# Optimization experiments

Hardware: AMD Instinct MI355X
Metric: run time of the kernel (lower is better)

Reference implementation:

```python
import jax, jax.numpy as jnp
import numpy as np

N1, N2, D = 8192, 8192, 128

def setup_inputs() -> dict:
    key = jax.random.key(0)
    k1, k2, k3, k4 = jax.random.split(key, 4)
    X1 = jax.random.normal(k1, (N1, D), dtype=jnp.float32)
    X2 = jax.random.normal(k2, (N2, D), dtype=jnp.float32)
    task1 = jax.random.randint(k3, (N1,), 0, 2, dtype=jnp.int32)
    task2 = jax.random.randint(k4, (N2,), 0, 2, dtype=jnp.int32)
    # learned parameters (init values match module defaults: lengthscale=1, output_variance=1, b=0)
    log_l = jnp.zeros((D,), dtype=jnp.float32)          # log(1)
    log_theta_l = jnp.zeros((1,), dtype=jnp.float32)    # log(1)
    b = jnp.zeros((1,), dtype=jnp.float32)
    return {"X1": X1, "X2": X2, "log_l": log_l, "log_theta_l": log_theta_l,
            "b": b, "task1": task1, "task2": task2}

def reference(X1, X2, log_l, log_theta_l, b, task1, task2):
    l = jnp.exp(log_l)                      # (D,) ARD lengthscales
    A = X1 / l                              # (N1, D)
    B = X2 / l                              # (N2, D)
    # sum((a-b)^2) = |a|^2 + |b|^2 - 2 a.b  -> GEMM form, no (N1,N2,D) intermediate
    sq_dist = (jnp.sum(A * A, axis=1)[:, None]
               + jnp.sum(B * B, axis=1)[None, :]
               - 2.0 * (A @ B.T))
    sq_dist = jnp.maximum(sq_dist, 0.0)
    K_base = jnp.exp(log_theta_l[0]) * jnp.exp(-0.5 * sq_dist)   # (N1, N2)
    # lambda = clip(2/(1+exp(b)) - 1, 0, 1)
    lam = jnp.clip(2.0 / (1.0 + jnp.exp(b[0])) - 1.0, 0.0, 1.0)
    diff_task = task1[:, None] != task2[None, :]                 # (N1, N2) bool
    K = K_base * jnp.where(diff_task, lam, 1.0)
    return K
```

## Files before the change

kernel.cpp:

```cpp
#include <hip/hip_runtime.h>
#include <stdint.h>

typedef float f32x4 __attribute__((ext_vector_type(4)));
typedef __bf16 bf16x8 __attribute__((ext_vector_type(8)));

#define N1 8192
#define N2 8192
#define DD 128
#define BK 32

__device__ __forceinline__ void gload_lds16(const void* g, void* l) {
    __builtin_amdgcn_global_load_lds(
        (const __attribute__((address_space(1))) uint32_t*)g,
        (__attribute__((address_space(3))) uint32_t*)l,
        16, 0, 0);
}

__global__ __launch_bounds__(256) void tgp_kernel(
    const float* __restrict__ X1, const float* __restrict__ X2,
    const float* __restrict__ log_l,
    const float* __restrict__ log_theta_l, const float* __restrict__ bparam,
    const int* __restrict__ t1, const int* __restrict__ t2,
    float* __restrict__ C)
{
    __shared__ __align__(128) char smem[65536 + 1536];
    float* const bounce = (float*)smem;
    float* const ils = (float*)(smem + 65536);
    float* const n1s = ils + 128;
    float* const n2s = ils + 256;

    const int t = threadIdx.x;
    const int lane = t & 63;
    const int wave = t >> 6;
    const int wr = wave >> 1, wc = wave & 1;
    const int lr = lane & 15, lg = lane >> 4;

    int wg = blockIdx.x;
    int swz = (wg & 7) * 512 + (wg >> 3);
    int tm = swz >> 6, tn = swz & 63;

    const float* Ag = X1 + (size_t)(tm * 128) * DD;
    const float* Bg = X2 + (size_t)(tn * 128) * DD;

    f32x4 acc[4][4];
    #pragma unroll
    for (int i = 0; i < 4; ++i)
        #pragma unroll
        for (int j = 0; j < 4; ++j) acc[i][j] = (f32x4){0.f, 0.f, 0.f, 0.f};

    #define STAGE(buf, kt)                                                          \
    {                                                                               \
        char* lb = smem + (buf) * 32768;                                            \
        int slot, row, ul;                                                          \
        slot = t;       row = slot >> 3; ul = (slot & 7) ^ (row & 7);               \
        gload_lds16(Ag + (size_t)row * DD + (kt) * BK + ul * 4, lb + slot * 16);    \
        gload_lds16(Bg + (size_t)row * DD + (kt) * BK + ul * 4, lb + 16384 + slot * 16); \
        slot = t + 256; row = slot >> 3; ul = (slot & 7) ^ (row & 7);               \
        gload_lds16(Ag + (size_t)row * DD + (kt) * BK + ul * 4, lb + slot * 16);    \
        gload_lds16(Bg + (size_t)row * DD + (kt) * BK + ul * 4, lb + 16384 + slot * 16); \
        slot = t + 512; row = slot >> 3; ul = (slot & 7) ^ (row & 7);               \
        gload_lds16(Ag + (size_t)row * DD + (kt) * BK + ul * 4, lb + slot * 16);    \
        gload_lds16(Bg + (size_t)row * DD + (kt) * BK + ul * 4, lb + 16384 + slot * 16); \
        slot = t + 768; row = slot >> 3; ul = (slot & 7) ^ (row & 7);               \
        gload_lds16(Ag + (size_t)row * DD + (kt) * BK + ul * 4, lb + slot * 16);    \
        gload_lds16(Bg + (size_t)row * DD + (kt) * BK + ul * 4, lb + 16384 + slot * 16); \
    }

    STAGE(0, 0);
    if (t < 128) ils[t] = __expf(-log_l[t]);
    __syncthreads();

    float nrm_acc = 0.f;
    const int nrow = t & 127;
    const int nroff = (t < 128) ? 0 : 16384;
    int cur = 0;

    for (int kt = 0; kt < 4; ++kt) {
        if (kt < 3) STAGE(cur ^ 1, kt + 1);

        const float* tA = (const float*)(smem + cur * 32768);
        const float* tB = tA + 4096;

        {
            const float* tp = (const float*)(smem + cur * 32768 + nroff);
            #pragma unroll
            for (int u = 0; u < 8; ++u) {
                int up = u ^ (nrow & 7);
                f32x4 x = *(const f32x4*)(tp + nrow * 32 + up * 4);
                f32x4 il = *(const f32x4*)(ils + kt * 32 + u * 4);
                f32x4 sx = x * il;
                nrm_acc += sx[0]*sx[0] + sx[1]*sx[1] + sx[2]*sx[2] + sx[3]*sx[3];
            }
        }

        float il8[8];
        {
            f32x4 i0 = *(const f32x4*)(ils + kt * 32 + lg * 8);
            f32x4 i1 = *(const f32x4*)(ils + kt * 32 + lg * 8 + 4);
            il8[0]=i0[0]; il8[1]=i0[1]; il8[2]=i0[2]; il8[3]=i0[3];
            il8[4]=i1[0]; il8[5]=i1[1]; il8[6]=i1[2]; il8[7]=i1[3];
        }
        bf16x8 ah[4], al[4], bh[4], bl[4];
        #pragma unroll
        for (int mi = 0; mi < 4; ++mi) {
            int row = wr * 64 + mi * 16 + lr;
            int p0 = (2 * lg) ^ (row & 7), p1 = (2 * lg + 1) ^ (row & 7);
            f32x4 x0 = *(const f32x4*)(tA + row * 32 + p0 * 4);
            f32x4 x1 = *(const f32x4*)(tA + row * 32 + p1 * 4);
            float sv[8] = {x0[0]*il8[0], x0[1]*il8[1], x0[2]*il8[2], x0[3]*il8[3],
                           x1[0]*il8[4], x1[1]*il8[5], x1[2]*il8[6], x1[3]*il8[7]};
            #pragma unroll
            for (int e = 0; e < 8; ++e) {
                __bf16 h = (__bf16)sv[e];
                ah[mi][e] = h;
                al[mi][e] = (__bf16)(sv[e] - (float)h);
            }
        }
        #pragma unroll
        for (int ni = 0; ni < 4; ++ni) {
            int row = wc * 64 + ni * 16 + lr;
            int p0 = (2 * lg) ^ (row & 7), p1 = (2 * lg + 1) ^ (row & 7);
            f32x4 x0 = *(const f32x4*)(tB + row * 32 + p0 * 4);
            f32x4 x1 = *(const f32x4*)(tB + row * 32 + p1 * 4);
            float sv[8] = {x0[0]*il8[0], x0[1]*il8[1], x0[2]*il8[2], x0[3]*il8[3],
                           x1[0]*il8[4], x1[1]*il8[5], x1[2]*il8[6], x1[3]*il8[7]};
            #pragma unroll
            for (int e = 0; e < 8; ++e) {
                __bf16 h = (__bf16)sv[e];
                bh[ni][e] = h;
                bl[ni][e] = (__bf16)(sv[e] - (float)h);
            }
        }

        #pragma unroll
        for (int mi = 0; mi < 4; ++mi)
            #pragma unroll
            for (int ni = 0; ni < 4; ++ni) {
                acc[mi][ni] = __builtin_amdgcn_mfma_f32_16x16x32_bf16(bh[ni], ah[mi], acc[mi][ni], 0, 0, 0);
                acc[mi][ni] = __builtin_amdgcn_mfma_f32_16x16x32_bf16(bh[ni], al[mi], acc[mi][ni], 0, 0, 0);
                acc[mi][ni] = __builtin_amdgcn_mfma_f32_16x16x32_bf16(bl[ni], ah[mi], acc[mi][ni], 0, 0, 0);
            }
        __syncthreads();
        cur ^= 1;
    }
    #undef STAGE

    if (t < 128) n1s[t] = nrm_acc; else n2s[t - 128] = nrm_acc;
    __syncthreads();

    float logt = log_theta_l[0];
    float bb = bparam[0];
    float lam = fminf(fmaxf(2.f / (1.f + __expf(bb)) - 1.f, 0.f), 1.f);
    int rbase = tm * 128, cbase = tn * 128;

    #pragma unroll
    for (int mi = 0; mi < 4; ++mi) {
        int rowl = wr * 64 + mi * 16 + lr;
        float n1v = n1s[rowl];
        int t1v = t1[rbase + rowl];
        #pragma unroll
        for (int ni = 0; ni < 4; ++ni) {
            int coll = wc * 64 + ni * 16 + lg * 4;
            f32x4 kv;
            #pragma unroll
            for (int r = 0; r < 4; ++r) {
                float dot = acc[mi][ni][r];
                float n2v = n2s[coll + r];
                int t2v = t2[cbase + coll + r];
                float s = fmaxf(n1v + n2v - 2.f * dot, 0.f);
                float k = __expf(fmaf(-0.5f, s, logt));
                if (t1v != t2v) k *= lam;
                kv[r] = k;
            }
            int phys = rowl * 128 + (coll ^ ((rowl & 7) << 2));
            *(f32x4*)(bounce + phys) = kv;
        }
    }
    __syncthreads();

    #pragma unroll
    for (int s2 = 0; s2 < 16; ++s2) {
        int lrow = s2 * 8 + (t >> 5);
        int lcol = (t & 31) * 4;
        int phys = lrow * 128 + (lcol ^ ((lrow & 7) << 2));
        f32x4 v = *(const f32x4*)(bounce + phys);
        *(f32x4*)(C + (size_t)(rbase + lrow) * N2 + (cbase + lcol)) = v;
    }
}

extern "C" void kernel_launch(void* const* d_in, const int* in_sizes, int n_in,
                              void* d_out, int out_size, void* d_ws, size_t ws_size,
                              hipStream_t stream)
{
    const float* X1 = (const float*)d_in[0];
    const float* X2 = (const float*)d_in[1];
    const float* log_l = (const float*)d_in[2];
    const float* log_theta = (const float*)d_in[3];
    const float* bp = (const float*)d_in[4];
    const int* t1 = (const int*)d_in[5];
    const int* t2 = (const int*)d_in[6];
    float* C = (float*)d_out;
    (void)d_ws; (void)ws_size; (void)in_sizes; (void)n_in; (void)out_size;

    tgp_kernel<<<4096, 256, 0, stream>>>(X1, X2, log_l, log_theta, bp, t1, t2, C);
}
```

Measured before the change: 117.5 us.

## Drop LDS staging; load operands directly from global and store output directly

Removes the double-buffered global-to-LDS async staging and the LDS bounce buffer used for coalesced output writes. Operands are now read straight from global into registers, row norms are computed per lane and reduced with wave shuffles, and results are written directly to global in MFMA layout. LDS use drops to a few hundred bytes and launch bounds request 3 blocks per SM, trading coalesced 512-byte row stores for 16-byte scattered stores and losing load/compute overlap.

```diff
diff --git a/kernel.cpp b/kernel.cpp
--- a/kernel.cpp
+++ b/kernel.cpp
@@ -4,43 +4,35 @@
 typedef float f32x4 __attribute__((ext_vector_type(4)));
 typedef __bf16 bf16x8 __attribute__((ext_vector_type(8)));
 
-#define N1 8192
-#define N2 8192
-#define DD 128
-#define BK 32
+#define NN 8192
+#define DDIM 128
 
-__device__ __forceinline__ void gload_lds16(const void* g, void* l) {
-    __builtin_amdgcn_global_load_lds(
-        (const __attribute__((address_space(1))) uint32_t*)g,
-        (__attribute__((address_space(3))) uint32_t*)l,
-        16, 0, 0);
-}
-
-__global__ __launch_bounds__(256) void tgp_kernel(
+__global__ __launch_bounds__(256, 3) void tgp_kernel(
     const float* __restrict__ X1, const float* __restrict__ X2,
     const float* __restrict__ log_l,
     const float* __restrict__ log_theta_l, const float* __restrict__ bparam,
-    const int* __restrict__ t1, const int* __restrict__ t2,
+    const int* __restrict__ task1, const int* __restrict__ task2,
     float* __restrict__ C)
 {
-    __shared__ __align__(128) char smem[65536 + 1536];
-    float* const bounce = (float*)smem;
-    float* const ils = (float*)(smem + 65536);
-    float* const n1s = ils + 128;
-    float* const n2s = ils + 256;
+    __shared__ float ils[128];
+    __shared__ float n1s[128];
+    __shared__ float n2s[128];
 
     const int t = threadIdx.x;
     const int lane = t & 63;
-    const int wave = t >> 6;
-    const int wr = wave >> 1, wc = wave & 1;
+    const int wv = t >> 6;
+    const int wr = wv >> 1, wc = wv & 1;
     const int lr = lane & 15, lg = lane >> 4;
 
     int wg = blockIdx.x;
     int swz = (wg & 7) * 512 + (wg >> 3);
     int tm = swz >> 6, tn = swz & 63;
 
-    const float* Ag = X1 + (size_t)(tm * 128) * DD;
-    const float* Bg = X2 + (size_t)(tn * 128) * DD;
+    const float* Ag = X1 + (size_t)tm * 128 * DDIM;
+    const float* Bg = X2 + (size_t)tn * 128 * DDIM;
+
+    if (t < 128) ils[t] = __expf(-log_l[t]);
+    __syncthreads();
 
     f32x4 acc[4][4];
     #pragma unroll
@@ -48,87 +40,50 @@
         #pragma unroll
         for (int j = 0; j < 4; ++j) acc[i][j] = (f32x4){0.f, 0.f, 0.f, 0.f};
 
-    #define STAGE(buf, kt)                                                          \
-    {                                                                               \
-        char* lb = smem + (buf) * 32768;                                            \
-        int slot, row, ul;                                                          \
-        slot = t;       row = slot >> 3; ul = (slot & 7) ^ (row & 7);               \
-        gload_lds16(Ag + (size_t)row * DD + (kt) * BK + ul * 4, lb + slot * 16);    \
-        gload_lds16(Bg + (size_t)row * DD + (kt) * BK + ul * 4, lb + 16384 + slot * 16); \
-        slot = t + 256; row = slot >> 3; ul = (slot & 7) ^ (row & 7);               \
-        gload_lds16(Ag + (size_t)row * DD + (kt) * BK + ul * 4, lb + slot * 16);    \
-        gload_lds16(Bg + (size_t)row * DD + (kt) * BK + ul * 4, lb + 16384 + slot * 16); \
-        slot = t + 512; row = slot >> 3; ul = (slot & 7) ^ (row & 7);               \
-        gload_lds16(Ag + (size_t)row * DD + (kt) * BK + ul * 4, lb + slot * 16);    \
-        gload_lds16(Bg + (size_t)row * DD + (kt) * BK + ul * 4, lb + 16384 + slot * 16); \
-        slot = t + 768; row = slot >> 3; ul = (slot & 7) ^ (row & 7);               \
-        gload_lds16(Ag + (size_t)row * DD + (kt) * BK + ul * 4, lb + slot * 16);    \
-        gload_lds16(Bg + (size_t)row * DD + (kt) * BK + ul * 4, lb + 16384 + slot * 16); \
-    }
+    float nA[4] = {0.f, 0.f, 0.f, 0.f};
+    float nB[4] = {0.f, 0.f, 0.f, 0.f};
 
-    STAGE(0, 0);
-    if (t < 128) ils[t] = __expf(-log_l[t]);
-    __syncthreads();
+    #pragma unroll
+    for (int c = 0; c < 4; ++c) {
+        f32x4 il0 = *(const f32x4*)(ils + c * 32 + lg * 8);
+        f32x4 il1 = *(const f32x4*)(ils + c * 32 + lg * 8 + 4);
 
-    float nrm_acc = 0.f;
-    const int nrow = t & 127;
-    const int nroff = (t < 128) ? 0 : 16384;
-    int cur = 0;
+        bf16x8 ah[4], al[4], bh[4], bl[4];
 
-    for (int kt = 0; kt < 4; ++kt) {
-        if (kt < 3) STAGE(cur ^ 1, kt + 1);
-
-        const float* tA = (const float*)(smem + cur * 32768);
-        const float* tB = tA + 4096;
-
-        {
-            const float* tp = (const float*)(smem + cur * 32768 + nroff);
-            #pragma unroll
-            for (int u = 0; u < 8; ++u) {
-                int up = u ^ (nrow & 7);
-                f32x4 x = *(const f32x4*)(tp + nrow * 32 + up * 4);
-                f32x4 il = *(const f32x4*)(ils + kt * 32 + u * 4);
-                f32x4 sx = x * il;
-                nrm_acc += sx[0]*sx[0] + sx[1]*sx[1] + sx[2]*sx[2] + sx[3]*sx[3];
-            }
-        }
-
-        float il8[8];
-        {
-            f32x4 i0 = *(const f32x4*)(ils + kt * 32 + lg * 8);
-            f32x4 i1 = *(const f32x4*)(ils + kt * 32 + lg * 8 + 4);
-            il8[0]=i0[0]; il8[1]=i0[1]; il8[2]=i0[2]; il8[3]=i0[3];
-            il8[4]=i1[0]; il8[5]=i1[1]; il8[6]=i1[2]; il8[7]=i1[3];
-        }
-        bf16x8 ah[4], al[4], bh[4], bl[4];
         #pragma unroll
         for (int mi = 0; mi < 4; ++mi) {
-            int row = wr * 64 + mi * 16 + lr;
-            int p0 = (2 * lg) ^ (row & 7), p1 = (2 * lg + 1) ^ (row & 7);
-            f32x4 x0 = *(const f32x4*)(tA + row * 32 + p0 * 4);
-            f32x4 x1 = *(const f32x4*)(tA + row * 32 + p1 * 4);
-            float sv[8] = {x0[0]*il8[0], x0[1]*il8[1], x0[2]*il8[2], x0[3]*il8[3],
-                           x1[0]*il8[4], x1[1]*il8[5], x1[2]*il8[6], x1[3]*il8[7]};
+            const float* p = Ag + (size_t)(wr * 64 + mi * 16 + lr) * DDIM + c * 32 + lg * 8;
+            f32x4 x0 = *(const f32x4*)p;
+            f32x4 x1 = *(const f32x4*)(p + 4);
+            x0 *= il0; x1 *= il1;
+            nA[mi] += x0[0]*x0[0] + x0[1]*x0[1] + x0[2]*x0[2] + x0[3]*x0[3]
+                    + x1[0]*x1[0] + x1[1]*x1[1] + x1[2]*x1[2] + x1[3]*x1[3];
             #pragma unroll
-            for (int e = 0; e < 8; ++e) {
-                __bf16 h = (__bf16)sv[e];
-                ah[mi][e] = h;
-                al[mi][e] = (__bf16)(sv[e] - (float)h);
+            for (int e = 0; e < 4; ++e) {
+                __bf16 h0 = (__bf16)x0[e];
+                ah[mi][e] = h0;
+                al[mi][e] = (__bf16)(x0[e] - (float)h0);
+                __bf16 h1 = (__bf16)x1[e];
+                ah[mi][e + 4] = h1;
+                al[mi][e + 4] = (__bf16)(x1[e] - (float)h1);
             }
         }
         #pragma unroll
         for (int ni = 0; ni < 4; ++ni) {
-            int row = wc * 64 + ni * 16 + lr;
-            int p0 = (2 * lg) ^ (row & 7), p1 = (2 * lg + 1) ^ (row & 7);
-            f32x4 x0 = *(const f32x4*)(tB + row * 32 + p0 * 4);
-            f32x4 x1 = *(const f32x4*)(tB + row * 32 + p1 * 4);
-            float sv[8] = {x0[0]*il8[0], x0[1]*il8[1], x0[2]*il8[2], x0[3]*il8[3],
-                           x1[0]*il8[4], x1[1]*il8[5], x1[2]*il8[6], x1[3]*il8[7]};
+            const float* p = Bg + (size_t)(wc * 64 + ni * 16 + lr) * DDIM + c * 32 + lg * 8;
+            f32x4 x0 = *(const f32x4*)p;
+            f32x4 x1 = *(const f32x4*)(p + 4);
+            x0 *= il0; x1 *= il1;
+            nB[ni] += x0[0]*x0[0] + x0[1]*x0[1] + x0[2]*x0[2] + x0[3]*x0[3]
+                    + x1[0]*x1[0] + x1[1]*x1[1] + x1[2]*x1[2] + x1[3]*x1[3];
             #pragma unroll
-            for (int e = 0; e < 8; ++e) {
-                __bf16 h = (__bf16)sv[e];
-                bh[ni][e] = h;
-                bl[ni][e] = (__bf16)(sv[e] - (float)h);
+            for (int e = 0; e < 4; ++e) {
+                __bf16 h0 = (__bf16)x0[e];
+                bh[ni][e] = h0;
+                bl[ni][e] = (__bf16)(x0[e] - (float)h0);
+                __bf16 h1 = (__bf16)x1[e];
+                bh[ni][e + 4] = h1;
+                bl[ni][e + 4] = (__bf16)(x1[e] - (float)h1);
             }
         }
 
@@ -140,12 +95,23 @@
                 acc[mi][ni] = __builtin_amdgcn_mfma_f32_16x16x32_bf16(bh[ni], al[mi], acc[mi][ni], 0, 0, 0);
                 acc[mi][ni] = __builtin_amdgcn_mfma_f32_16x16x32_bf16(bl[ni], ah[mi], acc[mi][ni], 0, 0, 0);
             }
-        __syncthreads();
-        cur ^= 1;
     }
-    #undef STAGE
 
-    if (t < 128) n1s[t] = nrm_acc; else n2s[t - 128] = nrm_acc;
+    #pragma unroll
+    for (int mi = 0; mi < 4; ++mi) {
+        nA[mi] += __shfl_xor(nA[mi], 16);
+        nA[mi] += __shfl_xor(nA[mi], 32);
+        nB[mi] += __shfl_xor(nB[mi], 16);
+        nB[mi] += __shfl_xor(nB[mi], 32);
+    }
+    if (wc == 0 && lg == 0) {
+        #pragma unroll
+        for (int mi = 0; mi < 4; ++mi) n1s[wr * 64 + mi * 16 + lr] = nA[mi];
+    }
+    if (wr == 0 && lg == 0) {
+        #pragma unroll
+        for (int ni = 0; ni < 4; ++ni) n2s[wc * 64 + ni * 16 + lr] = nB[ni];
+    }
     __syncthreads();
 
     float logt = log_theta_l[0];
@@ -157,34 +123,21 @@
     for (int mi = 0; mi < 4; ++mi) {
         int rowl = wr * 64 + mi * 16 + lr;
         float n1v = n1s[rowl];
-        int t1v = t1[rbase + rowl];
+        int t1v = task1[rbase + rowl];
         #pragma unroll
         for (int ni = 0; ni < 4; ++ni) {
             int coll = wc * 64 + ni * 16 + lg * 4;
             f32x4 kv;
             #pragma unroll
             for (int r = 0; r < 4; ++r) {
-                float dot = acc[mi][ni][r];
                 float n2v = n2s[coll + r];
-                int t2v = t2[cbase + coll + r];
-                float s = fmaxf(n1v + n2v - 2.f * dot, 0.f);
+                int t2v = task2[cbase + coll + r];
+                float s = fmaxf(n1v + n2v - 2.f * acc[mi][ni][r], 0.f);
                 float k = __expf(fmaf(-0.5f, s, logt));
-                if (t1v != t2v) k *= lam;
-                kv[r] = k;
+                kv[r] = (t1v != t2v) ? k * lam : k;
             }
-            int phys = rowl * 128 + (coll ^ ((rowl & 7) << 2));
-            *(f32x4*)(bounce + phys) = kv;
+            *(f32x4*)(C + (size_t)(rbase + rowl) * NN + cbase + coll) = kv;
         }
-    }
-    __syncthreads();
-
-    #pragma unroll
-    for (int s2 = 0; s2 < 16; ++s2) {
-        int lrow = s2 * 8 + (t >> 5);
-        int lcol = (t & 31) * 4;
-        int phys = lrow * 128 + (lcol ^ ((lrow & 7) << 2));
-        f32x4 v = *(const f32x4*)(bounce + phys);
-        *(f32x4*)(C + (size_t)(rbase + lrow) * N2 + (cbase + lcol)) = v;
     }
 }
 
```

Result: slower. 222.9 us (+89.6%).
